# Kernel tuning notes

Hardware: AMD Instinct MI355X
Metric: run time of the kernel (lower is better)

Reference implementation:

```python
import jax, jax.numpy as jnp
import numpy as np
from math import sqrt

B, LQ, LKV = 4, 1024, 1024
QD = KD = VD = 1024
MODEL_DIM = 1024
H = 16
HD = MODEL_DIM // H  # per-head model_dim = 64


def setup_inputs() -> dict:
    key = jax.random.key(0)
    ks = jax.random.split(key, 10)
    s = 0.02
    return {
        "queries": jax.random.normal(ks[0], (B, LQ, QD), jnp.float32),
        "context": jax.random.normal(ks[1], (B, LKV, KD), jnp.float32),
        # stacked per-head linear weights (torch Linear: y = x @ W.T + b); store as [H, in, out]
        "Wq": jax.random.normal(ks[2], (H, QD, HD), jnp.float32) * s,
        "bq": jax.random.normal(ks[3], (H, HD), jnp.float32) * s,
        "Wk": jax.random.normal(ks[4], (KD, HD * 1 * H), jnp.float32).reshape(H, KD, HD) * s,
        "bk": jax.random.normal(ks[5], (H, HD), jnp.float32) * s,
        "Wv": jax.random.normal(ks[6], (H, VD, HD), jnp.float32) * s,
        "bv": jax.random.normal(ks[7], (H, HD), jnp.float32) * s,
        "Wo": jax.random.normal(ks[8], (H * HD, MODEL_DIM), jnp.float32) * s,
        "bo": jax.random.normal(ks[9], (MODEL_DIM,), jnp.float32) * s,
    }


def reference(queries, context, Wq, bq, Wk, bk, Wv, bv, Wo, bo):
    # queries: [B,Lq,Dq]; context: [B,Lkv,Dk]
    # Per-head projections, batched over heads (equivalent to the torch per-head loop).
    q = jnp.einsum("bld,hdm->bhlm", queries, Wq) + bq[None, :, None, :]  # [B,H,Lq,hd]
    k = jnp.einsum("bld,hdm->bhlm", context, Wk) + bk[None, :, None, :]  # [B,H,Lkv,hd]
    v = jnp.einsum("bld,hdm->bhlm", context, Wv) + bv[None, :, None, :]  # [B,H,Lkv,hd]

    scale = 1.0 / sqrt(HD)
    scores = jnp.einsum("bhqd,bhkd->bhqk", q, k) * scale  # [B,H,Lq,Lkv]
    att = jax.nn.softmax(scores, axis=-1)
    head_out = jnp.einsum("bhqk,bhkd->bhqd", att, v)  # [B,H,Lq,hd]

    # torch concatenates heads along the last dim in head order 0..H-1
    multi = head_out.transpose(0, 2, 1, 3).reshape(B, LQ, H * HD)
    residual = q.transpose(0, 2, 1, 3).reshape(B, LQ, H * HD)

    out = multi @ Wo + bo  # [B,Lq,model_dim]
    return out, residual
```

## Files before the change

kernel.cpp:

```cpp
#include <hip/hip_runtime.h>
#include <hip/hip_bf16.h>


typedef unsigned short u16;
typedef __attribute__((ext_vector_type(8))) short short8;
typedef __attribute__((ext_vector_type(4))) float f32x4;

__device__ __forceinline__ float bf2f(u16 u) {
    union { unsigned int i; float f; } c;
    c.i = ((unsigned int)u) << 16;
    return c.f;
}

__device__ __forceinline__ u16 f2bf(float f) {
    unsigned int x = __float_as_uint(f);
    unsigned int r = (x + 0x7fffu + ((x >> 16) & 1u)) >> 16;
    return (u16)r;
}

__device__ __forceinline__ void glds16(u16* lds, const u16* g) {
    __builtin_amdgcn_global_load_lds(
        (const __attribute__((address_space(1))) void*)g,
        (__attribute__((address_space(3))) void*)lds, 16, 0, 0);
}

#define FENCE() asm volatile("" ::: "memory")
#define BAR() do { FENCE(); __builtin_amdgcn_s_barrier(); FENCE(); } while (0)
#define WAIT_VM8() do { asm volatile("s_waitcnt vmcnt(8)" ::: "memory"); \
                        __builtin_amdgcn_sched_barrier(0); } while (0)
#define WAIT_VM6() do { asm volatile("s_waitcnt vmcnt(6)" ::: "memory"); \
                        __builtin_amdgcn_sched_barrier(0); } while (0)
#define WAIT_VM4() do { asm volatile("s_waitcnt vmcnt(4)" ::: "memory"); \
                        __builtin_amdgcn_sched_barrier(0); } while (0)
#define WAIT_VM0() do { asm volatile("s_waitcnt vmcnt(0)" ::: "memory"); \
                        __builtin_amdgcn_sched_barrier(0); } while (0)

__global__ __launch_bounds__(256) void prep(
    const float* __restrict__ q, const float* __restrict__ ctx,
    const float* __restrict__ Wq, const float* __restrict__ Wk,
    const float* __restrict__ Wv, const float* __restrict__ Wo,
    u16* __restrict__ Aq, u16* __restrict__ Ac,
    u16* __restrict__ Wqt, u16* __restrict__ Wkt,
    u16* __restrict__ Wvt, u16* __restrict__ Wot)
{
    __shared__ float ls[64][65];
    const int t = threadIdx.x;
    int bid = blockIdx.x;

    if (bid < 4096) {
        const float* in = (bid < 2048) ? q : ctx;
        u16* out = (bid < 2048) ? Aq : Ac;
        size_t i = ((size_t)(bid & 2047) * 256 + t) * 8;
        float4 v0 = *(const float4*)(in + i);
        float4 v1 = *(const float4*)(in + i + 4);
        short8 p;
        p[0] = (short)f2bf(v0.x); p[1] = (short)f2bf(v0.y);
        p[2] = (short)f2bf(v0.z); p[3] = (short)f2bf(v0.w);
        p[4] = (short)f2bf(v1.x); p[5] = (short)f2bf(v1.y);
        p[6] = (short)f2bf(v1.z); p[7] = (short)f2bf(v1.w);
        *(short8*)(out + i) = p;
        return;
    }
    bid -= 4096;
    const float* in; u16* out; int C; size_t moff; int rt, ct;
    if (bid < 768) {
        const int m = bid >> 8, idx = bid & 255;
        in = (m == 0) ? Wq : (m == 1) ? Wk : Wv;
        out = (m == 0) ? Wqt : (m == 1) ? Wkt : Wvt;
        C = 64; rt = (idx & 15) * 64; ct = 0; moff = (size_t)(idx >> 4) * 65536;
    } else {
        const int idx = bid - 768;
        in = Wo; out = Wot; C = 1024; moff = 0;
        rt = (idx & 15) * 64; ct = (idx >> 4) * 64;
    }
    #pragma unroll
    for (int i = 0; i < 4; ++i) {
        int s = i * 256 + t;
        int row = s >> 4, chunk = s & 15;
        float4 v = *(const float4*)(in + moff + (size_t)(rt + row) * C + ct + chunk * 4);
        ls[row][chunk * 4 + 0] = v.x;
        ls[row][chunk * 4 + 1] = v.y;
        ls[row][chunk * 4 + 2] = v.z;
        ls[row][chunk * 4 + 3] = v.w;
    }
    __syncthreads();
    #pragma unroll
    for (int i = 0; i < 2; ++i) {
        int s = i * 256 + t;
        int n = s >> 3, kc = s & 7;
        short8 p;
        #pragma unroll
        for (int j = 0; j < 8; ++j) p[j] = (short)f2bf(ls[kc * 8 + j][n]);
        *(short8*)(out + moff + (size_t)(ct + n) * 1024 + rt + kc * 8) = p;
    }
}

__global__ __launch_bounds__(512) void gemm_qkv2(
    const u16* __restrict__ Aq, const u16* __restrict__ Ac,
    const u16* __restrict__ Wqt, const u16* __restrict__ Wkt,
    const u16* __restrict__ Wvt,
    const float* __restrict__ bq, const float* __restrict__ bk,
    const float* __restrict__ bv,
    u16* __restrict__ qws, u16* __restrict__ kws, u16* __restrict__ vtws)
{
    __shared__ u16 lds[2][2][256 * 64];

    const int tid = threadIdx.x;
    const int w = tid >> 6, lane = tid & 63;
    const int wr = w >> 2, wc = w & 3;
    const int quad = lane >> 4, c = lane & 15, cx = c & 7;
    const int sr = tid >> 3;
    const int gch = (tid & 7) ^ (sr & 7);

    const int f = blockIdx.x;
    const int xcd = f & 7, r = f >> 3;
    const int z = r >> 3;
    const int mt = xcd * 2 + ((r >> 2) & 1);
    const int nt = r & 3;
    const int m0 = mt * 256, n0 = nt * 256;

    const u16* A = (z == 0) ? Aq : Ac;
    const u16* Wt = (z == 0) ? Wqt : (z == 1) ? Wkt : Wvt;
    const float* bias = (z == 0) ? bq : (z == 1) ? bk : bv;

    const u16* gAt = A + (size_t)(m0 + sr) * 1024 + gch * 8;
    const u16* gBt = Wt + (size_t)(n0 + sr) * 1024 + gch * 8;

    auto stage = [&](int par, int t) {
        #pragma unroll
        for (int i = 0; i < 4; ++i) {
            glds16(&lds[par][0][(i * 64 + w * 8) * 64],
                   gAt + (size_t)(i * 64) * 1024 + t * 64);
            glds16(&lds[par][1][(i * 64 + w * 8) * 64],
                   gBt + (size_t)(i * 64) * 1024 + t * 64);
        }
    };

    f32x4 acc[8][4] = {};
    short8 aq[4][2], bA[2][2], bB[2][2];

    auto ldA = [&](int par, int mh) {
        #pragma unroll
        for (int mf = 0; mf < 4; ++mf)
            #pragma unroll
            for (int ks = 0; ks < 2; ++ks)
                aq[mf][ks] = *(const short8*)&lds[par][0][
                    (wr * 128 + mh * 64 + mf * 16 + c) * 64 + (((ks * 4 + quad) ^ cx) * 8)];
    };
    auto ldB = [&](int par, int nh, short8 (&bq_)[2][2]) {
        #pragma unroll
        for (int nf = 0; nf < 2; ++nf)
            #pragma unroll
            for (int ks = 0; ks < 2; ++ks)
                bq_[nf][ks] = *(const short8*)&lds[par][1][
                    (wc * 64 + nh * 32 + nf * 16 + c) * 64 + (((ks * 4 + quad) ^ cx) * 8)];
    };
    auto mma = [&](int mh, int nh, short8 (&bq_)[2][2]) {
        #pragma unroll
        for (int mf = 0; mf < 4; ++mf)
            #pragma unroll
            for (int nf = 0; nf < 2; ++nf)
                #pragma unroll
                for (int ks = 0; ks < 2; ++ks)
                    acc[mh * 4 + mf][nh * 2 + nf] =
                        __builtin_amdgcn_mfma_f32_16x16x32_bf16(
                            aq[mf][ks], bq_[nf][ks], acc[mh * 4 + mf][nh * 2 + nf], 0, 0, 0);
    };

    stage(0, 0);
    stage(1, 1);
    #pragma unroll 1
    for (int i = 0; i < 16; ++i) {
        const int cur = i & 1;
        if (i < 15) { WAIT_VM8(); } else { WAIT_VM0(); }
        BAR();
        ldA(cur, 0);
        ldB(cur, 0, bA);
        mma(0, 0, bA);
        ldB(cur, 1, bB);
        mma(0, 1, bB);
        ldA(cur, 1);
        mma(1, 1, bB);
        mma(1, 0, bA);
        BAR();
        if (i < 14) stage(cur, i + 2);
    }

    const int h = nt * 4 + wc;
    const int b = m0 >> 10;
    const int lbase = (m0 & 1023) + wr * 128;

    float bb[4];
    #pragma unroll
    for (int cn = 0; cn < 4; ++cn)
        bb[cn] = bias[h * 64 + (cn >> 1) * 32 + (cn & 1) * 16 + c];

    if (z < 2) {
        u16* dst = (z == 0) ? qws : kws;
        const float scale = (z == 0) ? 0.125f : 1.0f;
        u16* dbase = dst + (size_t)(b * 16 + h) * 1024 * 64;
        #pragma unroll
        for (int mi = 0; mi < 8; ++mi) {
            const int ro = (mi >> 2) * 64 + (mi & 3) * 16;
            const int rowb = lbase + ro + quad * 4;
            #pragma unroll
            for (int rr = 0; rr < 4; ++rr) {
                u16* drow = dbase + (size_t)(rowb + rr) * 64;
                #pragma unroll
                for (int cn = 0; cn < 4; ++cn) {
                    const int hd = (cn >> 1) * 32 + (cn & 1) * 16 + c;
                    drow[hd] = f2bf((acc[mi][cn][rr] + bb[cn]) * scale);
                }
            }
        }
    } else {
        u16* dbase = vtws + (size_t)(b * 16 + h) * 64 * 1024;
        #pragma unroll
        for (int mi = 0; mi < 8; ++mi) {
            const int ro = (mi >> 2) * 64 + (mi & 3) * 16;
            const int l0 = lbase + ro + quad * 4;
            #pragma unroll
            for (int cn = 0; cn < 4; ++cn) {
                const int hd = (cn >> 1) * 32 + (cn & 1) * 16 + c;
                ushort4 pk;
                pk.x = f2bf(acc[mi][cn][0] + bb[cn]);
                pk.y = f2bf(acc[mi][cn][1] + bb[cn]);
                pk.z = f2bf(acc[mi][cn][2] + bb[cn]);
                pk.w = f2bf(acc[mi][cn][3] + bb[cn]);
                *(ushort4*)(dbase + (size_t)hd * 1024 + l0) = pk;
            }
        }
    }
}

__global__ __launch_bounds__(256) void gemm_out(
    const u16* __restrict__ A, const u16* __restrict__ Wot,
    const float* __restrict__ bo, float* __restrict__ out)
{
    __shared__ u16 As[2][128 * 64];
    __shared__ u16 Bs[2][64 * 64];
    const int f = blockIdx.x;
    const int xcd = f & 7, k = f >> 3;
    const int m0 = (xcd * 4 + (k & 3)) * 128;
    const int n0 = (k >> 2) * 64;
    const int t = threadIdx.x;
    const int w = t >> 6, lane = t & 63;
    const int quad = lane >> 4, c = lane & 15;
    const int cx = c & 7;

    const int sr = w * 8 + (lane >> 3);
    const int gch = (lane & 7) ^ ((lane >> 3) & 7);
    const u16* gA = A + (size_t)(m0 + sr) * 1024 + gch * 8;
    const u16* gB = Wot + (size_t)(n0 + sr) * 1024 + gch * 8;

    const int arow = (w >> 1) * 64 + c;
    const int brow = (w & 1) * 32 + c;

    auto stage = [&](int par, int kt) {
        #pragma unroll
        for (int i = 0; i < 4; ++i)
            glds16(As[par] + (i * 32 + w * 8) * 64, gA + (size_t)i * 32 * 1024 + kt);
        #pragma unroll
        for (int i = 0; i < 2; ++i)
            glds16(Bs[par] + (i * 32 + w * 8) * 64, gB + (size_t)i * 32 * 1024 + kt);
    };

    f32x4 acc[4][2] = {};
    stage(0, 0);
    stage(1, 64);
    #pragma unroll 1
    for (int i = 0; i < 16; ++i) {
        const int cur = i & 1;
        if (i < 15) { WAIT_VM6(); } else { WAIT_VM0(); }
        BAR();
        #pragma unroll
        for (int kh = 0; kh < 2; ++kh) {
            const int ch = (kh * 4 + quad);
            short8 af[4], bf[2];
            #pragma unroll
            for (int rs = 0; rs < 4; ++rs)
                af[rs] = *(const short8*)(As[cur] + (arow + rs * 16) * 64 + (ch ^ cx) * 8);
            #pragma unroll
            for (int cs = 0; cs < 2; ++cs)
                bf[cs] = *(const short8*)(Bs[cur] + (brow + cs * 16) * 64 + (ch ^ cx) * 8);
            #pragma unroll
            for (int rs = 0; rs < 4; ++rs)
                #pragma unroll
                for (int cs = 0; cs < 2; ++cs)
                    acc[rs][cs] = __builtin_amdgcn_mfma_f32_16x16x32_bf16(
                        af[rs], bf[cs], acc[rs][cs], 0, 0, 0);
        }
        BAR();
        if (i < 14) stage(cur, (i + 2) * 64);
    }

    const int nb = n0 + (w & 1) * 32;
    float bb[2];
    #pragma unroll
    for (int cs = 0; cs < 2; ++cs) bb[cs] = bo[nb + cs * 16 + c];

    #pragma unroll
    for (int rs = 0; rs < 4; ++rs) {
        #pragma unroll
        for (int r = 0; r < 4; ++r) {
            const int row = m0 + (w >> 1) * 64 + rs * 16 + quad * 4 + r;
            float* orow = out + (size_t)row * 1024 + nb;
            #pragma unroll
            for (int cs = 0; cs < 2; ++cs)
                orow[cs * 16 + c] = acc[rs][cs][r] + bb[cs];
        }
    }
}

__global__ __launch_bounds__(256) void attn_mfma(
    const u16* __restrict__ qws, const u16* __restrict__ kws,
    const u16* __restrict__ vtws, u16* __restrict__ multi,
    float* __restrict__ resid)
{
    __shared__ u16 Ks[2][64 * 64];
    __shared__ u16 Vs[2][64 * 64];
    __shared__ u16 Ps[4][16 * 64];
    const int t = threadIdx.x;
    const int wave = t >> 6, lane = t & 63;
    const int quad = lane >> 4, c = lane & 15;
    const int cx = c & 7;
    const int f = blockIdx.x;
    const int xcd = f & 7, j = f >> 3;
    const int bh = xcd * 8 + (j & 7);
    const int qt = j >> 3;
    const int b = bh >> 4, h = bh & 15;
    const int q0 = qt * 128 + wave * 32;

    const u16* qb = qws + ((size_t)bh * 1024 + q0) * 64;
    const u16* kb = kws + (size_t)bh * 65536;
    const u16* vb = vtws + (size_t)bh * 65536;

    short8 qa[2][2];
    #pragma unroll
    for (int rb = 0; rb < 2; ++rb) {
        qa[rb][0] = *(const short8*)(qb + (size_t)(rb * 16 + c) * 64 + quad * 8);
        qa[rb][1] = *(const short8*)(qb + (size_t)(rb * 16 + c) * 64 + 32 + quad * 8);
    }

    const int srow = wave * 16 + (lane >> 3);
    const int gch = (lane & 7) ^ ((lane >> 3) & 7);
    const u16* gK0 = kb + (size_t)srow * 64 + gch * 8;
    const u16* gK1 = kb + (size_t)(srow + 8) * 64 + gch * 8;
    const u16* gV0 = vb + (size_t)srow * 1024 + gch * 8;
    const u16* gV1 = vb + (size_t)(srow + 8) * 1024 + gch * 8;

    auto stage = [&](int par, int kt) {
        glds16(Ks[par] + (wave * 16) * 64,     gK0 + (size_t)kt * 64);
        glds16(Ks[par] + (wave * 16 + 8) * 64, gK1 + (size_t)kt * 64);
        glds16(Vs[par] + (wave * 16) * 64,     gV0 + kt);
        glds16(Vs[par] + (wave * 16 + 8) * 64, gV1 + kt);
    };

    f32x4 O[2][4] = {};
    float ps[2][4] = {};
    u16* pw = &Ps[wave][0];

    stage(0, 0);
    stage(1, 64);

    #pragma unroll 1
    for (int i = 0; i < 16; ++i) {
        const int cur = i & 1;
        if (i < 15) { WAIT_VM4(); } else { WAIT_VM0(); }
        BAR();

        const u16* Kc = Ks[cur];
        const u16* Vc = Vs[cur];

        short8 kf[4][2], vf[4][2];
        #pragma unroll
        for (int nt = 0; nt < 4; ++nt) {
            const u16* kr = Kc + (nt * 16 + c) * 64;
            kf[nt][0] = *(const short8*)(kr + ((quad ^ cx)) * 8);
            kf[nt][1] = *(const short8*)(kr + (((4 + quad) ^ cx)) * 8);
            const u16* vr = Vc + (nt * 16 + c) * 64;
            vf[nt][0] = *(const short8*)(vr + ((quad ^ cx)) * 8);
            vf[nt][1] = *(const short8*)(vr + (((4 + quad) ^ cx)) * 8);
        }

        #pragma unroll
        for (int rb = 0; rb < 2; ++rb) {
            f32x4 s[4];
            __builtin_amdgcn_s_setprio(1);
            #pragma unroll
            for (int nt = 0; nt < 4; ++nt) {
                f32x4 z = {};
                z = __builtin_amdgcn_mfma_f32_16x16x32_bf16(qa[rb][0], kf[nt][0], z, 0, 0, 0);
                z = __builtin_amdgcn_mfma_f32_16x16x32_bf16(qa[rb][1], kf[nt][1], z, 0, 0, 0);
                s[nt] = z;
            }
            __builtin_amdgcn_s_setprio(0);

            #pragma unroll
            for (int nt = 0; nt < 4; ++nt)
                #pragma unroll
                for (int r = 0; r < 4; ++r) {
                    float p = __expf(s[nt][r]);
                    ps[rb][r] += p;
                    const int prow = quad * 4 + r;
                    pw[prow * 64 + (((nt * 2 + (c >> 3)) ^ (prow & 7)) * 8) + (c & 7)]
                        = (u16)(__float_as_uint(p) >> 16);
                }
            short8 pa0 = *(const short8*)(pw + c * 64 + ((quad ^ cx)) * 8);
            short8 pa1 = *(const short8*)(pw + c * 64 + (((4 + quad) ^ cx)) * 8);

            __builtin_amdgcn_s_setprio(1);
            #pragma unroll
            for (int nt = 0; nt < 4; ++nt) {
                O[rb][nt] = __builtin_amdgcn_mfma_f32_16x16x32_bf16(pa0, vf[nt][0], O[rb][nt], 0, 0, 0);
                O[rb][nt] = __builtin_amdgcn_mfma_f32_16x16x32_bf16(pa1, vf[nt][1], O[rb][nt], 0, 0, 0);
            }
            __builtin_amdgcn_s_setprio(0);
        }

        BAR();
        if (i < 14) stage(cur, (i + 2) * 64);
    }

    #pragma unroll
    for (int rb = 0; rb < 2; ++rb) {
        float inv[4];
        #pragma unroll
        for (int r = 0; r < 4; ++r) {
            float sum = ps[rb][r];
            sum += __shfl_xor(sum, 1);
            sum += __shfl_xor(sum, 2);
            sum += __shfl_xor(sum, 4);
            sum += __shfl_xor(sum, 8);
            inv[r] = 1.0f / sum;
        }
        u16* ob = multi + ((size_t)b * 1024 + q0 + rb * 16 + quad * 4) * 1024 + h * 64 + c;
        #pragma unroll
        for (int r = 0; r < 4; ++r) {
            u16* orow = ob + (size_t)r * 1024;
            orow[0]  = f2bf(O[rb][0][r] * inv[r]);
            orow[16] = f2bf(O[rb][1][r] * inv[r]);
            orow[32] = f2bf(O[rb][2][r] * inv[r]);
            orow[48] = f2bf(O[rb][3][r] * inv[r]);
        }

        float* rr = resid + ((size_t)b * 1024 + q0 + rb * 16 + c) * 1024 + h * 64;
        #pragma unroll
        for (int jj = 0; jj < 8; ++jj) {
            rr[quad * 8 + jj]      = bf2f((u16)qa[rb][0][jj]) * 8.0f;
            rr[32 + quad * 8 + jj] = bf2f((u16)qa[rb][1][jj]) * 8.0f;
        }
    }
}

extern "C" void kernel_launch(void* const* d_in, const int* in_sizes, int n_in,
                              void* d_out, int out_size, void* d_ws, size_t ws_size,
                              hipStream_t stream) {
    const float* queries = (const float*)d_in[0];
    const float* context = (const float*)d_in[1];
    const float* Wq = (const float*)d_in[2];
    const float* bq = (const float*)d_in[3];
    const float* Wk = (const float*)d_in[4];
    const float* bk = (const float*)d_in[5];
    const float* Wv = (const float*)d_in[6];
    const float* bv = (const float*)d_in[7];
    const float* Wo = (const float*)d_in[8];
    const float* bo = (const float*)d_in[9];

    float* out = (float*)d_out;
    float* resid = out + (size_t)4 * 1024 * 1024;

    const size_t M1 = 1024 * 1024;
    u16* Aq   = (u16*)d_ws;
    u16* Ac   = Aq + 4 * M1;
    u16* Wqt  = Ac + 4 * M1;
    u16* Wkt  = Wqt + M1;
    u16* Wvt  = Wkt + M1;
    u16* Wot  = Wvt + M1;
    u16* qws  = Wot + M1;
    u16* kws  = qws + 4 * M1;
    u16* vtws = kws + 4 * M1;
    u16* mws  = vtws + 4 * M1;

    prep<<<5120, 256, 0, stream>>>(queries, context, Wq, Wk, Wv, Wo,
                                   Aq, Ac, Wqt, Wkt, Wvt, Wot);
    gemm_qkv2<<<192, 512, 0, stream>>>(Aq, Ac, Wqt, Wkt, Wvt,
                                       bq, bk, bv, qws, kws, vtws);
    attn_mfma<<<512, 256, 0, stream>>>(qws, kws, vtws, mws, resid);
    gemm_out<<<512, 256, 0, stream>>>(mws, Wot, bo, out);
}
```

Before: 188.4 us.

## Retile QKV GEMM to 128x128 tiles with 256-thread blocks

Replaces the 256x256-tile, 512-thread QKV projection GEMM with a 128x128-tile, 256-thread version launched as 768 blocks, with two blocks per CU allowed. The old grid of 192 blocks left many of the 256 CUs idle; the smaller tile is meant to fill the machine and allow more latency hiding. The cost is lower data reuse per tile, hence more global and LDS traffic per FLOP. The fragment loads are also simplified into a single load-then-MFMA phase per K step.

```diff
diff --git a/kernel.cpp b/kernel.cpp
--- a/kernel.cpp
+++ b/kernel.cpp
@@ -95,7 +95,7 @@
     }
 }
 
-__global__ __launch_bounds__(512) void gemm_qkv2(
+__global__ __launch_bounds__(256, 2) void gemm_qkv3(
     const u16* __restrict__ Aq, const u16* __restrict__ Ac,
     const u16* __restrict__ Wqt, const u16* __restrict__ Wkt,
     const u16* __restrict__ Wvt,
@@ -103,69 +103,39 @@
     const float* __restrict__ bv,
     u16* __restrict__ qws, u16* __restrict__ kws, u16* __restrict__ vtws)
 {
-    __shared__ u16 lds[2][2][256 * 64];
-
-    const int tid = threadIdx.x;
-    const int w = tid >> 6, lane = tid & 63;
-    const int wr = w >> 2, wc = w & 3;
+    __shared__ u16 As[2][128 * 64];
+    __shared__ u16 Bs[2][128 * 64];
+    const int t = threadIdx.x;
+    const int w = t >> 6, lane = t & 63;
+    const int wr = w >> 1, wc = w & 1;
     const int quad = lane >> 4, c = lane & 15, cx = c & 7;
-    const int sr = tid >> 3;
-    const int gch = (tid & 7) ^ (sr & 7);
 
     const int f = blockIdx.x;
     const int xcd = f & 7, r = f >> 3;
-    const int z = r >> 3;
-    const int mt = xcd * 2 + ((r >> 2) & 1);
-    const int nt = r & 3;
-    const int m0 = mt * 256, n0 = nt * 256;
+    const int z = r >> 5;
+    const int rr_ = r & 31;
+    const int mt = xcd * 4 + (rr_ & 3);
+    const int nt = rr_ >> 2;
+    const int m0 = mt * 128, n0 = nt * 128;
 
     const u16* A = (z == 0) ? Aq : Ac;
     const u16* Wt = (z == 0) ? Wqt : (z == 1) ? Wkt : Wvt;
     const float* bias = (z == 0) ? bq : (z == 1) ? bk : bv;
 
-    const u16* gAt = A + (size_t)(m0 + sr) * 1024 + gch * 8;
-    const u16* gBt = Wt + (size_t)(n0 + sr) * 1024 + gch * 8;
-
-    auto stage = [&](int par, int t) {
+    const int sr = w * 8 + (lane >> 3);
+    const int gch = (lane & 7) ^ ((lane >> 3) & 7);
+    const u16* gA = A + (size_t)(m0 + sr) * 1024 + gch * 8;
+    const u16* gB = Wt + (size_t)(n0 + sr) * 1024 + gch * 8;
+
+    auto stage = [&](int par, int tk) {
         #pragma unroll
         for (int i = 0; i < 4; ++i) {
-            glds16(&lds[par][0][(i * 64 + w * 8) * 64],
-                   gAt + (size_t)(i * 64) * 1024 + t * 64);
-            glds16(&lds[par][1][(i * 64 + w * 8) * 64],
-                   gBt + (size_t)(i * 64) * 1024 + t * 64);
+            glds16(As[par] + (i * 32 + w * 8) * 64, gA + (size_t)(i * 32) * 1024 + tk * 64);
+            glds16(Bs[par] + (i * 32 + w * 8) * 64, gB + (size_t)(i * 32) * 1024 + tk * 64);
         }
     };
 
-    f32x4 acc[8][4] = {};
-    short8 aq[4][2], bA[2][2], bB[2][2];
-
-    auto ldA = [&](int par, int mh) {
-        #pragma unroll
-        for (int mf = 0; mf < 4; ++mf)
-            #pragma unroll
-            for (int ks = 0; ks < 2; ++ks)
-                aq[mf][ks] = *(const short8*)&lds[par][0][
-                    (wr * 128 + mh * 64 + mf * 16 + c) * 64 + (((ks * 4 + quad) ^ cx) * 8)];
-    };
-    auto ldB = [&](int par, int nh, short8 (&bq_)[2][2]) {
-        #pragma unroll
-        for (int nf = 0; nf < 2; ++nf)
-            #pragma unroll
-            for (int ks = 0; ks < 2; ++ks)
-                bq_[nf][ks] = *(const short8*)&lds[par][1][
-                    (wc * 64 + nh * 32 + nf * 16 + c) * 64 + (((ks * 4 + quad) ^ cx) * 8)];
-    };
-    auto mma = [&](int mh, int nh, short8 (&bq_)[2][2]) {
-        #pragma unroll
-        for (int mf = 0; mf < 4; ++mf)
-            #pragma unroll
-            for (int nf = 0; nf < 2; ++nf)
-                #pragma unroll
-                for (int ks = 0; ks < 2; ++ks)
-                    acc[mh * 4 + mf][nh * 2 + nf] =
-                        __builtin_amdgcn_mfma_f32_16x16x32_bf16(
-                            aq[mf][ks], bq_[nf][ks], acc[mh * 4 + mf][nh * 2 + nf], 0, 0, 0);
-    };
+    f32x4 acc[4][4] = {};
 
     stage(0, 0);
     stage(1, 1);
@@ -174,59 +144,67 @@
         const int cur = i & 1;
         if (i < 15) { WAIT_VM8(); } else { WAIT_VM0(); }
         BAR();
-        ldA(cur, 0);
-        ldB(cur, 0, bA);
-        mma(0, 0, bA);
-        ldB(cur, 1, bB);
-        mma(0, 1, bB);
-        ldA(cur, 1);
-        mma(1, 1, bB);
-        mma(1, 0, bA);
+        short8 af[4][2], bf[4][2];
+        #pragma unroll
+        for (int mf = 0; mf < 4; ++mf)
+            #pragma unroll
+            for (int ks = 0; ks < 2; ++ks)
+                af[mf][ks] = *(const short8*)&As[cur][
+                    (wr * 64 + mf * 16 + c) * 64 + (((ks * 4 + quad) ^ cx) * 8)];
+        #pragma unroll
+        for (int nf = 0; nf < 4; ++nf)
+            #pragma unroll
+            for (int ks = 0; ks < 2; ++ks)
+                bf[nf][ks] = *(const short8*)&Bs[cur][
+                    (wc * 64 + nf * 16 + c) * 64 + (((ks * 4 + quad) ^ cx) * 8)];
+        #pragma unroll
+        for (int mf = 0; mf < 4; ++mf)
+            #pragma unroll
+            for (int nf = 0; nf < 4; ++nf)
+                #pragma unroll
+                for (int ks = 0; ks < 2; ++ks)
+                    acc[mf][nf] = __builtin_amdgcn_mfma_f32_16x16x32_bf16(
+                        af[mf][ks], bf[nf][ks], acc[mf][nf], 0, 0, 0);
         BAR();
         if (i < 14) stage(cur, i + 2);
     }
 
-    const int h = nt * 4 + wc;
+    const int h = nt * 2 + wc;
     const int b = m0 >> 10;
-    const int lbase = (m0 & 1023) + wr * 128;
+    const int lbase = (m0 & 1023) + wr * 64;
 
     float bb[4];
     #pragma unroll
-    for (int cn = 0; cn < 4; ++cn)
-        bb[cn] = bias[h * 64 + (cn >> 1) * 32 + (cn & 1) * 16 + c];
+    for (int nf = 0; nf < 4; ++nf) bb[nf] = bias[h * 64 + nf * 16 + c];
 
     if (z < 2) {
         u16* dst = (z == 0) ? qws : kws;
         const float scale = (z == 0) ? 0.125f : 1.0f;
         u16* dbase = dst + (size_t)(b * 16 + h) * 1024 * 64;
         #pragma unroll
-        for (int mi = 0; mi < 8; ++mi) {
-            const int ro = (mi >> 2) * 64 + (mi & 3) * 16;
-            const int rowb = lbase + ro + quad * 4;
-            #pragma unroll
-            for (int rr = 0; rr < 4; ++rr) {
-                u16* drow = dbase + (size_t)(rowb + rr) * 64;
+        for (int mf = 0; mf < 4; ++mf) {
+            const int rowb = lbase + mf * 16 + quad * 4;
+            #pragma unroll
+            for (int rw = 0; rw < 4; ++rw) {
+                u16* drow = dbase + (size_t)(rowb + rw) * 64;
                 #pragma unroll
-                for (int cn = 0; cn < 4; ++cn) {
-                    const int hd = (cn >> 1) * 32 + (cn & 1) * 16 + c;
-                    drow[hd] = f2bf((acc[mi][cn][rr] + bb[cn]) * scale);
-                }
+                for (int nf = 0; nf < 4; ++nf)
+                    drow[nf * 16 + c] = f2bf((acc[mf][nf][rw] + bb[nf]) * scale);
             }
         }
     } else {
         u16* dbase = vtws + (size_t)(b * 16 + h) * 64 * 1024;
         #pragma unroll
-        for (int mi = 0; mi < 8; ++mi) {
-            const int ro = (mi >> 2) * 64 + (mi & 3) * 16;
-            const int l0 = lbase + ro + quad * 4;
-            #pragma unroll
-            for (int cn = 0; cn < 4; ++cn) {
-                const int hd = (cn >> 1) * 32 + (cn & 1) * 16 + c;
+        for (int mf = 0; mf < 4; ++mf) {
+            const int l0 = lbase + mf * 16 + quad * 4;
+            #pragma unroll
+            for (int nf = 0; nf < 4; ++nf) {
+                const int hd = nf * 16 + c;
                 ushort4 pk;
-                pk.x = f2bf(acc[mi][cn][0] + bb[cn]);
-                pk.y = f2bf(acc[mi][cn][1] + bb[cn]);
-                pk.z = f2bf(acc[mi][cn][2] + bb[cn]);
-                pk.w = f2bf(acc[mi][cn][3] + bb[cn]);
+                pk.x = f2bf(acc[mf][nf][0] + bb[nf]);
+                pk.y = f2bf(acc[mf][nf][1] + bb[nf]);
+                pk.z = f2bf(acc[mf][nf][2] + bb[nf]);
+                pk.w = f2bf(acc[mf][nf][3] + bb[nf]);
                 *(ushort4*)(dbase + (size_t)hd * 1024 + l0) = pk;
             }
         }
@@ -484,7 +462,7 @@
 
     prep<<<5120, 256, 0, stream>>>(queries, context, Wq, Wk, Wv, Wo,
                                    Aq, Ac, Wqt, Wkt, Wvt, Wot);
-    gemm_qkv2<<<192, 512, 0, stream>>>(Aq, Ac, Wqt, Wkt, Wvt,
+    gemm_qkv3<<<768, 256, 0, stream>>>(Aq, Ac, Wqt, Wkt, Wvt,
                                        bq, bk, bv, qws, kws, vtws);
     attn_mfma<<<512, 256, 0, stream>>>(qws, kws, vtws, mws, resid);
     gemm_out<<<512, 256, 0, stream>>>(mws, Wot, bo, out);
```

Result: no change. 189.0 us (+0.3%).
